# Kernel optimization log

Measured on AMD Instinct MI355X. Metric: run time of the kernel, lower is better.

## Reference

```python
import jax, jax.numpy as jnp
import numpy as np

N_WORDS = 8192   # total words across all concepts
L = 24           # chars per word (padded)
D = 256          # word_vec_d
H = 8            # attention heads
DFF = 1024
VOCAB = 128
N_CONCEPTS = 1024
MAXW = 16        # max_words
GROUPS = 4       # n_names: 4 equal groups of concepts


def setup_inputs() -> dict:
    key = jax.random.key(0)
    ks = jax.random.split(key, 9)
    rng = np.random.default_rng(0)
    # char tokens in [1, VOCAB), ragged word lengths in [4, L], tail = 0 (pad)
    vals = rng.integers(1, VOCAB, size=(N_WORDS, L))
    lens = rng.integers(4, L + 1, size=(N_WORDS,))
    inputs = np.where(np.arange(L)[None, :] < lens[:, None], vals, 0)
    # ragged words-per-concept: alternate 4 / 12 -> sums to N_WORDS, <= MAXW
    counts = np.where(np.arange(N_CONCEPTS) % 2 == 0, 4, 12)
    concept_id = np.repeat(np.arange(N_CONCEPTS), counts)
    word_pos = np.concatenate([np.arange(c) for c in counts])

    def w(k, shape):
        return 0.02 * jax.random.normal(k, shape, jnp.float32)

    return {
        "inputs": jnp.asarray(inputs, jnp.int32),
        "concept_id": jnp.asarray(concept_id, jnp.int32),
        "word_pos": jnp.asarray(word_pos, jnp.int32),
        "n_concepts": N_CONCEPTS,
        "n_names": GROUPS,
        "we_emb": w(ks[0], (VOCAB, D)),
        "we_qkv": w(ks[1], (D, 3 * D)),
        "we_o": w(ks[2], (D, D)),
        "we_ff1": w(ks[3], (D, DFF)),
        "we_ff2": w(ks[4], (DFF, D)),
        "ne_qkv": w(ks[5], (D, 3 * D)),
        "ne_o": w(ks[6], (D, D)),
        "ne_ff1": w(ks[7], (D, DFF)),
        "ne_ff2": w(ks[8], (DFF, D)),
    }


def _ln(x):
    m = x.mean(-1, keepdims=True)
    v = ((x - m) ** 2).mean(-1, keepdims=True)
    return (x - m) * jax.lax.rsqrt(v + 1e-5)


def _mha(x, wqkv, wo, key_pad=None):
    n, l, d = x.shape
    hd = d // H
    q, k, v = jnp.split(x @ wqkv, 3, axis=-1)
    q = q.reshape(n, l, H, hd)
    k = k.reshape(n, l, H, hd)
    v = v.reshape(n, l, H, hd)
    s = jnp.einsum('nqhd,nkhd->nhqk', q, k) / jnp.sqrt(jnp.asarray(hd, x.dtype))
    if key_pad is not None:
        s = jnp.where(key_pad[:, None, None, :], -1e9, s)
    a = jax.nn.softmax(s, axis=-1)
    o = jnp.einsum('nhqk,nkhd->nqhd', a, v).reshape(n, l, d)
    return o @ wo


def _block(x, wqkv, wo, w1, w2, key_pad=None):
    h = _ln(x + _mha(x, wqkv, wo, key_pad))
    return _ln(h + jax.nn.relu(h @ w1) @ w2)


def reference(inputs, concept_id, word_pos, n_concepts, n_names,
              we_emb, we_qkv, we_o, we_ff1, we_ff2,
              ne_qkv, ne_o, ne_ff1, ne_ff2):
    pad_mask = inputs == 0  # [N_WORDS, L]
    x = we_emb[inputs]      # [N_WORDS, L, D]
    word_ft = _block(x, we_qkv, we_o, we_ff1, we_ff2, pad_mask)
    # masked mean over chars -> one vector per word
    np_mask = (~pad_mask)[..., None].astype(word_ft.dtype)  # [N_WORDS, L, 1]
    name_vec = (word_ft * np_mask).sum(1) / np_mask.sum(1)   # [N_WORDS, D]
    # ragged -> padded: one scatter instead of per-sample torch.cat
    padded = jnp.zeros((n_concepts, MAXW, name_vec.shape[-1]), name_vec.dtype)
    padded = padded.at[concept_id, word_pos].set(name_vec)   # [n_concepts, MAXW, D]
    name_ft = _block(padded, ne_qkv, ne_o, ne_ff1, ne_ff2)
    row_pad = (padded == 0).all(-1, keepdims=True)           # all-zero rows = pad words
    name_ft = jnp.where(row_pad, jnp.zeros((), name_ft.dtype), name_ft)
    counts = (name_ft != 0).sum(1).astype(name_ft.dtype)     # [n_concepts, D]
    pooled = name_ft.sum(1) / counts                         # [n_concepts, D]
    return tuple(jnp.split(pooled, n_names, axis=0))
```

## Files before the change

### kernel.cpp

```cpp
#include <hip/hip_runtime.h>
#include <hip/hip_bf16.h>

#define NWORDS 8192
#define LW 24
#define DIM 256
#define NHEAD 8
#define DFF 1024
#define NCONC 1024
#define MAXW 16
#define TN (NCONC * MAXW)

typedef float floatx4 __attribute__((ext_vector_type(4)));
typedef short shortx8 __attribute__((ext_vector_type(8)));

__device__ __forceinline__ float bf2f(ushort u) {
  union { uint u; float f; } v; v.u = ((uint)u) << 16; return v.f;
}
__device__ __forceinline__ ushort f2bf(float f) {
  union { float f; uint u; } v; v.f = f;
  return (ushort)((v.u + 0x7FFFu + ((v.u >> 16) & 1u)) >> 16);
}

__device__ __forceinline__ void load_lds16(const ushort* gsrc, ushort* lds) {
  __builtin_amdgcn_global_load_lds((const __attribute__((address_space(1))) void*)gsrc,
                                   (__attribute__((address_space(3))) void*)lds, 16, 0, 0);
}

#define WAIT_VM0() __builtin_amdgcn_s_waitcnt(0x0F70)
#define WAIT_LGKM0() __builtin_amdgcn_s_waitcnt(0xC07F)

#define STAGE_COL(lane) ((((lane) & 3) ^ (((lane) >> 3) & 3)) * 8)
#define FRAG_OFF(row, quad) (((row) * 32) + ((((quad) ^ (((row) >> 1) & 3))) * 8))

__global__ __launch_bounds__(256) void wprep(const float* __restrict__ W,
                                             ushort* __restrict__ WT, int K, int N) {
  int idx = blockIdx.x * 256 + threadIdx.x;
  if (idx < K * N) {
    int k = idx / N, n = idx % N;
    WT[n * K + k] = f2bf(W[idx]);
  }
}

__global__ __launch_bounds__(256) void embed4(const int* __restrict__ inputs,
                                              const float* __restrict__ we_emb,
                                              ushort* __restrict__ x, int ntok) {
  int idx = blockIdx.x * 256 + threadIdx.x;
  int t = idx >> 6, d = (idx & 63) * 4;
  if (t < ntok) {
    const float4 f = *(const float4*)&we_emb[inputs[t] * DIM + d];
    uint2 o;
    o.x = (uint)f2bf(f.x) | ((uint)f2bf(f.y) << 16);
    o.y = (uint)f2bf(f.z) | ((uint)f2bf(f.w) << 16);
    *(uint2*)&x[(size_t)t * DIM + d] = o;
  }
}

template <bool LN>
__global__ __launch_bounds__(256, 2) void gemm_tok64(const ushort* __restrict__ A, int lda,
                                                     const ushort* __restrict__ BT,
                                                     const ushort* __restrict__ RES,
                                                     ushort* __restrict__ C, int ldc) {
  __shared__ __align__(16) ushort As[8 * 64 * 32];
  __shared__ __align__(16) ushort Wb[256 * 32];
  __shared__ float red1[64 * 4];
  __shared__ float red2[64 * 4];
  const int tid = threadIdx.x;
  const int w = tid >> 6, lane = tid & 63;
  const int quad = lane >> 4, l16 = lane & 15;
  const long m0 = (long)blockIdx.y * 64;
  const long nb = (long)blockIdx.x * 256;
  const int srow = lane >> 2;
  const int scol = STAGE_COL(lane);
  const int wc = w * 64;

#pragma unroll
  for (int t = 0; t < 8; t++) {
    int p = 2 * w + t / 4, ii = t % 4;
    load_lds16(&A[(m0 + ii * 16 + srow) * lda + p * 32 + scol], &As[p * 2048 + (ii * 16) * 32]);
  }
#pragma unroll
  for (int ii = 0; ii < 4; ii++)
    load_lds16(&BT[(nb + wc + ii * 16 + srow) * 256 + scol], &Wb[(wc + ii * 16) * 32]);
  __syncthreads();

  floatx4 acc[4][4] = {};
#pragma unroll 1
  for (int p = 0; p < 8; p++) {
    WAIT_VM0();
    shortx8 a[4], b[4];
#pragma unroll
    for (int j = 0; j < 4; j++)
      b[j] = *(const shortx8*)&Wb[FRAG_OFF(wc + j * 16 + l16, quad)];
    WAIT_LGKM0();
    if (p < 7) {
#pragma unroll
      for (int ii = 0; ii < 4; ii++)
        load_lds16(&BT[(nb + wc + ii * 16 + srow) * 256 + (p + 1) * 32 + scol],
                   &Wb[(wc + ii * 16) * 32]);
    }
#pragma unroll
    for (int i = 0; i < 4; i++)
      a[i] = *(const shortx8*)&As[p * 2048 + FRAG_OFF(i * 16 + l16, quad)];
#pragma unroll
    for (int i = 0; i < 4; i++)
#pragma unroll
      for (int j = 0; j < 4; j++)
        acc[i][j] = __builtin_amdgcn_mfma_f32_16x16x32_bf16(a[i], b[j], acc[i][j], 0, 0, 0);
  }

  if (!LN) {
#pragma unroll
    for (int i = 0; i < 4; i++)
#pragma unroll
      for (int j = 0; j < 4; j++)
#pragma unroll
        for (int r = 0; r < 4; r++) {
          long m = m0 + i * 16 + quad * 4 + r;
          C[m * ldc + nb + wc + j * 16 + l16] = f2bf(acc[i][j][r]);
        }
    return;
  }

#pragma unroll
  for (int i = 0; i < 4; i++)
#pragma unroll
    for (int r = 0; r < 4; r++) {
      int row = i * 16 + quad * 4 + r;
      float s1 = 0.f, s2 = 0.f;
#pragma unroll
      for (int j = 0; j < 4; j++) {
        float v = acc[i][j][r] + bf2f(RES[(m0 + row) * 256 + wc + j * 16 + l16]);
        acc[i][j][r] = v;
        s1 += v;
        s2 += v * v;
      }
#pragma unroll
      for (int off = 1; off < 16; off <<= 1) {
        s1 += __shfl_xor(s1, off);
        s2 += __shfl_xor(s2, off);
      }
      if (l16 == 0) { red1[row * 4 + w] = s1; red2[row * 4 + w] = s2; }
    }
  __syncthreads();
#pragma unroll
  for (int i = 0; i < 4; i++)
#pragma unroll
    for (int r = 0; r < 4; r++) {
      int row = i * 16 + quad * 4 + r;
      float s1 = red1[row * 4] + red1[row * 4 + 1] + red1[row * 4 + 2] + red1[row * 4 + 3];
      float s2 = red2[row * 4] + red2[row * 4 + 1] + red2[row * 4 + 2] + red2[row * 4 + 3];
      float mean = s1 * (1.f / 256.f);
      float rstd = rsqrtf(s2 * (1.f / 256.f) - mean * mean + 1e-5f);
#pragma unroll
      for (int j = 0; j < 4; j++)
        C[(m0 + row) * 256 + wc + j * 16 + l16] = f2bf((acc[i][j][r] - mean) * rstd);
    }
}

__global__ __launch_bounds__(256, 2) void ffn_fused(const ushort* __restrict__ H,
                                                    const ushort* __restrict__ W1T,
                                                    const ushort* __restrict__ W2T,
                                                    ushort* __restrict__ C,
                                                    int M) {
  __shared__ __align__(16) ushort As[8 * 64 * 32];
  __shared__ __align__(16) ushort Ss[8 * 64 * 32];
  __shared__ __align__(16) ushort Wb[256 * 32];
  const int tid = threadIdx.x;
  const int w = tid >> 6, lane = tid & 63;
  const int quad = lane >> 4, l16 = lane & 15;
  const long m0 = (long)blockIdx.x * 64;
  const int srow = lane >> 2;
  const int scol = STAGE_COL(lane);

#pragma unroll
  for (int t = 0; t < 8; t++) {
    int p = 2 * w + t / 4, ii = t % 4;
    load_lds16(&H[(m0 + ii * 16 + srow) * 256 + p * 32 + scol], &As[(p * 2048) + (ii * 16) * 32]);
  }
#pragma unroll
  for (int ii = 0; ii < 4; ii++)
    load_lds16(&W1T[(long)(w * 64 + ii * 16 + srow) * 256 + scol], &Wb[(w * 64 + ii * 16) * 32]);
  __syncthreads();

  floatx4 acc2[4][4] = {};
  for (int m = 0; m < 4; m++) {
    floatx4 acc1[4][4] = {};
    if (m > 0) {
#pragma unroll
      for (int ii = 0; ii < 4; ii++)
        load_lds16(&W1T[(long)(m * 256 + w * 64 + ii * 16 + srow) * 256 + scol],
                   &Wb[(w * 64 + ii * 16) * 32]);
    }
#pragma unroll 1
    for (int p = 0; p < 8; p++) {
      WAIT_VM0();
      shortx8 a[4], b[4];
#pragma unroll
      for (int i = 0; i < 4; i++)
        a[i] = *(const shortx8*)&Wb[FRAG_OFF(w * 64 + i * 16 + l16, quad)];
      WAIT_LGKM0();
      if (p < 7) {
#pragma unroll
        for (int ii = 0; ii < 4; ii++)
          load_lds16(&W1T[(long)(m * 256 + w * 64 + ii * 16 + srow) * 256 + (p + 1) * 32 + scol],
                     &Wb[(w * 64 + ii * 16) * 32]);
      }
#pragma unroll
      for (int j = 0; j < 4; j++)
        b[j] = *(const shortx8*)&As[p * 2048 + FRAG_OFF(j * 16 + l16, quad)];
#pragma unroll
      for (int i = 0; i < 4; i++)
#pragma unroll
        for (int j = 0; j < 4; j++)
          acc1[i][j] = __builtin_amdgcn_mfma_f32_16x16x32_bf16(a[i], b[j], acc1[i][j], 0, 0, 0);
    }
    __syncthreads();
#pragma unroll
    for (int i = 0; i < 4; i++) {
      int fb = w * 64 + i * 16 + quad * 4;
      int pf = fb >> 5, c = (fb >> 3) & 3, off = fb & 7;
#pragma unroll
      for (int j = 0; j < 4; j++) {
        int tok = j * 16 + l16;
        ushort4 pk;
        pk.x = f2bf(fmaxf(acc1[i][j][0], 0.f));
        pk.y = f2bf(fmaxf(acc1[i][j][1], 0.f));
        pk.z = f2bf(fmaxf(acc1[i][j][2], 0.f));
        pk.w = f2bf(fmaxf(acc1[i][j][3], 0.f));
        *(ushort4*)&Ss[(pf * 64 + tok) * 32 + ((c ^ ((tok >> 1) & 3)) << 3) + off] = pk;
      }
    }
    __syncthreads();
#pragma unroll
    for (int jj = 0; jj < 4; jj++)
      load_lds16(&W2T[(long)(w * 64 + jj * 16 + srow) * 1024 + m * 256 + scol],
                 &Wb[(w * 64 + jj * 16) * 32]);
#pragma unroll 1
    for (int p = 0; p < 8; p++) {
      WAIT_VM0();
      shortx8 a[4], b[4];
#pragma unroll
      for (int j = 0; j < 4; j++)
        b[j] = *(const shortx8*)&Wb[FRAG_OFF(w * 64 + j * 16 + l16, quad)];
      WAIT_LGKM0();
      if (p < 7) {
#pragma unroll
        for (int jj = 0; jj < 4; jj++)
          load_lds16(&W2T[(long)(w * 64 + jj * 16 + srow) * 1024 + m * 256 + (p + 1) * 32 + scol],
                     &Wb[(w * 64 + jj * 16) * 32]);
      }
#pragma unroll
      for (int i = 0; i < 4; i++)
        a[i] = *(const shortx8*)&Ss[p * 2048 + FRAG_OFF(i * 16 + l16, quad)];
#pragma unroll
      for (int i = 0; i < 4; i++)
#pragma unroll
        for (int j = 0; j < 4; j++)
          acc2[i][j] = __builtin_amdgcn_mfma_f32_16x16x32_bf16(a[i], b[j], acc2[i][j], 0, 0, 0);
    }
  }
  __syncthreads();

  float* red1 = (float*)Ss;
  float* red2 = red1 + 256;
  const int wc = w * 64;
#pragma unroll
  for (int i = 0; i < 4; i++)
#pragma unroll
    for (int r = 0; r < 4; r++) {
      int row = i * 16 + quad * 4 + r;
      float s1 = 0.f, s2 = 0.f;
#pragma unroll
      for (int j = 0; j < 4; j++) {
        float v = acc2[i][j][r] + bf2f(H[(m0 + row) * 256 + wc + j * 16 + l16]);
        acc2[i][j][r] = v;
        s1 += v;
        s2 += v * v;
      }
#pragma unroll
      for (int off = 1; off < 16; off <<= 1) {
        s1 += __shfl_xor(s1, off);
        s2 += __shfl_xor(s2, off);
      }
      if (l16 == 0) { red1[row * 4 + w] = s1; red2[row * 4 + w] = s2; }
    }
  __syncthreads();
#pragma unroll
  for (int i = 0; i < 4; i++)
#pragma unroll
    for (int r = 0; r < 4; r++) {
      int row = i * 16 + quad * 4 + r;
      float s1 = red1[row * 4] + red1[row * 4 + 1] + red1[row * 4 + 2] + red1[row * 4 + 3];
      float s2 = red2[row * 4] + red2[row * 4 + 1] + red2[row * 4 + 2] + red2[row * 4 + 3];
      float mean = s1 * (1.f / 256.f);
      float rstd = rsqrtf(s2 * (1.f / 256.f) - mean * mean + 1e-5f);
      if (m0 + row < M) {
#pragma unroll
        for (int j = 0; j < 4; j++)
          C[(m0 + row) * 256 + wc + j * 16 + l16] = f2bf((acc2[i][j][r] - mean) * rstd);
      }
    }
}

template <int LSEQ, bool MASKED>
__global__ __launch_bounds__(256) void attn(const int* __restrict__ inputs,
                                            ushort* __restrict__ qkv) {
  __shared__ ushort Qs[LSEQ * 256];
  __shared__ ushort Ks[LSEQ * 256];
  __shared__ ushort Vs[LSEQ * 256];
  __shared__ float pads[LSEQ];
  const int blk = blockIdx.x;
  const int tid = threadIdx.x;
  ushort* base = qkv + (size_t)blk * LSEQ * 768;
  const uint4* src = (const uint4*)base;
  for (int i = tid; i < LSEQ * 96; i += 256) {
    int c = i / 96, part = i % 96;
    uint4 val = src[c * 96 + part];
    int sect = part >> 5, off = part & 31;
    ushort* dst = (sect == 0) ? Qs : (sect == 1 ? Ks : Vs);
    *(uint4*)&dst[c * 256 + off * 8] = val;
  }
  if (MASKED) {
    if (tid < LSEQ) pads[tid] = (inputs[blk * LSEQ + tid] == 0) ? 1.f : 0.f;
  }
  __syncthreads();
  if (tid < LSEQ * NHEAD) {
    const int i = tid % LSEQ, hh = tid / LSEQ;
    const int hb = hh * 32;
    float q[32];
    {
      const uint4* qr = (const uint4*)&Qs[i * 256 + hb];
#pragma unroll
      for (int u = 0; u < 4; u++) {
        uint4 ch = qr[u];
        const ushort* us = (const ushort*)&ch;
#pragma unroll
        for (int d = 0; d < 8; d++) q[u * 8 + d] = bf2f(us[d]);
      }
    }
    float s[LSEQ];
    float mx = -3e38f;
#pragma unroll
    for (int j = 0; j < LSEQ; j++) {
      const uint4* kr = (const uint4*)&Ks[j * 256 + hb];
      float a = 0.f;
#pragma unroll
      for (int u = 0; u < 4; u++) {
        uint4 ch = kr[u];
        const ushort* us = (const ushort*)&ch;
#pragma unroll
        for (int d = 0; d < 8; d++) a += q[u * 8 + d] * bf2f(us[d]);
      }
      a *= 0.17677669529663687f;
      if (MASKED && pads[j] != 0.f) a = -1e9f;
      s[j] = a;
      mx = fmaxf(mx, a);
    }
    float den = 0.f;
#pragma unroll
    for (int j = 0; j < LSEQ; j++) { s[j] = __expf(s[j] - mx); den += s[j]; }
    float inv = 1.f / den;
    float o[32] = {};
#pragma unroll
    for (int j = 0; j < LSEQ; j++) {
      float a = s[j] * inv;
      const uint4* vr = (const uint4*)&Vs[j * 256 + hb];
#pragma unroll
      for (int u = 0; u < 4; u++) {
        uint4 ch = vr[u];
        const ushort* us = (const ushort*)&ch;
#pragma unroll
        for (int d = 0; d < 8; d++) o[u * 8 + d] += a * bf2f(us[d]);
      }
    }
    ushort* orow = base + (size_t)i * 768 + hb;
#pragma unroll
    for (int d = 0; d < 32; d++) orow[d] = f2bf(o[d]);
  }
}

__global__ __launch_bounds__(256) void pool_scatter(const ushort* __restrict__ ft,
                                                    const int* __restrict__ inputs,
                                                    const int* __restrict__ cid,
                                                    const int* __restrict__ wpos,
                                                    ushort* __restrict__ padded,
                                                    int* __restrict__ flags) {
  int w = blockIdx.x, d = threadIdx.x;
  float s = 0.f;
  int cnt = 0;
  for (int c = 0; c < LW; c++) {
    if (inputs[w * LW + c] != 0) {
      s += bf2f(ft[((size_t)w * LW + c) * DIM + d]);
      cnt++;
    }
  }
  int slot = cid[w] * MAXW + wpos[w];
  padded[(size_t)slot * DIM + d] = f2bf(s / (float)cnt);
  if (d == 0) flags[slot] = 1;
}

__global__ __launch_bounds__(256) void final_pool(const ushort* __restrict__ nft,
                                                  const int* __restrict__ flags,
                                                  float* __restrict__ out) {
  int n = blockIdx.x, d = threadIdx.x;
  float s = 0.f;
  int cnt = 0;
  for (int wd = 0; wd < MAXW; wd++) {
    if (flags[n * MAXW + wd]) {
      s += bf2f(nft[((size_t)n * MAXW + wd) * DIM + d]);
      cnt++;
    }
  }
  out[n * DIM + d] = s / (float)cnt;
}

extern "C" void kernel_launch(void* const* d_in, const int* in_sizes, int n_in,
                              void* d_out, int out_size, void* d_ws, size_t ws_size,
                              hipStream_t stream) {
  const int* inputs = (const int*)d_in[0];
  const int* cid = (const int*)d_in[1];
  const int* wpos = (const int*)d_in[2];
  const float* we_emb = (const float*)d_in[5];
  const float* we_qkv = (const float*)d_in[6];
  const float* we_o = (const float*)d_in[7];
  const float* we_ff1 = (const float*)d_in[8];
  const float* we_ff2 = (const float*)d_in[9];
  const float* ne_qkv = (const float*)d_in[10];
  const float* ne_o = (const float*)d_in[11];
  const float* ne_ff1 = (const float*)d_in[12];
  const float* ne_ff2 = (const float*)d_in[13];
  float* out = (float*)d_out;

  int chunks = 4;
  if (ws_size >= 515000000UL) chunks = 1;
  else if (ws_size >= 263258112UL) chunks = 2;
  const int wpc = NWORDS / chunks;
  const int tpc = wpc * LW;

  const size_t X = (size_t)tpc * DIM * 2;
  const size_t Q = (size_t)tpc * 768 * 2;

  char* base = (char*)d_ws;
  ushort* x = (ushort*)(base);
  ushort* qkv = (ushort*)(base + X);
  ushort* h = (ushort*)(base + X + Q);
  ushort* ft = qkv;
  size_t pend = X + Q + X;
  ushort* padded = (ushort*)(base + pend);
  int* flags = (int*)(base + pend + 8388608);
  ushort* wT = (ushort*)(base + pend + 8454144);
  ushort* nqkv = (ushort*)(base);
  ushort* nh = (ushort*)(base + 25165824);
  ushort* nft = (ushort*)(base + 33554432);

  ushort* wqkvT = wT;
  ushort* woT = wT + 196608;
  ushort* wff1T = wT + 262144;
  ushort* wff2T = wT + 524288;
  ushort* nqkvT = wT + 786432;
  ushort* neoT = wT + 983040;
  ushort* neff1T = wT + 1048576;
  ushort* neff2T = wT + 1310720;

  wprep<<<768, 256, 0, stream>>>(we_qkv, wqkvT, 256, 768);
  wprep<<<256, 256, 0, stream>>>(we_o, woT, 256, 256);
  wprep<<<1024, 256, 0, stream>>>(we_ff1, wff1T, 256, 1024);
  wprep<<<1024, 256, 0, stream>>>(we_ff2, wff2T, 1024, 256);
  wprep<<<768, 256, 0, stream>>>(ne_qkv, nqkvT, 256, 768);
  wprep<<<256, 256, 0, stream>>>(ne_o, neoT, 256, 256);
  wprep<<<1024, 256, 0, stream>>>(ne_ff1, neff1T, 256, 1024);
  wprep<<<1024, 256, 0, stream>>>(ne_ff2, neff2T, 1024, 256);

  (void)hipMemsetAsync(padded, 0, (size_t)TN * DIM * 2, stream);
  (void)hipMemsetAsync(flags, 0, TN * 4, stream);

  for (int c = 0; c < chunks; c++) {
    const int* in_c = inputs + (size_t)c * wpc * LW;
    const int* cid_c = cid + (size_t)c * wpc;
    const int* wpos_c = wpos + (size_t)c * wpc;

    embed4<<<tpc / 4, 256, 0, stream>>>(in_c, we_emb, x, tpc);
    {
      dim3 g(3, tpc / 64);
      gemm_tok64<false><<<g, 256, 0, stream>>>(x, 256, wqkvT, nullptr, qkv, 768);
    }
    attn<24, true><<<wpc, 256, 0, stream>>>(in_c, qkv);
    {
      dim3 g(1, tpc / 64);
      gemm_tok64<true><<<g, 256, 0, stream>>>(qkv, 768, woT, x, h, 256);
    }
    ffn_fused<<<tpc / 64, 256, 0, stream>>>(h, wff1T, wff2T, ft, tpc);
    pool_scatter<<<wpc, 256, 0, stream>>>(ft, in_c, cid_c, wpos_c, padded, flags);
  }

  {
    dim3 g(3, TN / 64);
    gemm_tok64<false><<<g, 256, 0, stream>>>(padded, 256, nqkvT, nullptr, nqkv, 768);
  }
  attn<16, false><<<NCONC, 256, 0, stream>>>(nullptr, nqkv);
  {
    dim3 g(1, TN / 64);
    gemm_tok64<true><<<g, 256, 0, stream>>>(nqkv, 768, neoT, padded, nh, 256);
  }
  ffn_fused<<<TN / 64, 256, 0, stream>>>(nh, neff1T, neff2T, nft, TN);
  final_pool<<<NCONC, 256, 0, stream>>>(nft, flags, out);
}
```

Baseline: 972.8 us.

## Load FFN weight fragments directly into registers with double-buffered prefetch

The fused FFN kernel no longer stages W1/W2 weight tiles through a shared LDS buffer. Each wave now loads its own weight fragments straight from global memory into a two-slot register double buffer, prefetching two k-steps ahead across both GEMM phases and across m iterations. This drops the per-step vmcnt waits, the LDS writes and reads for weights, and some block-wide __syncthreads, which are replaced by raw s_barrier. In exchange it uses more VGPRs, issues uncoalesced 16-byte global loads, and fully unrolls the inner loops.

```diff
diff --git a/kernel.cpp b/kernel.cpp
--- a/kernel.cpp
+++ b/kernel.cpp
@@ -164,47 +164,42 @@
                                                     int M) {
   __shared__ __align__(16) ushort As[8 * 64 * 32];
   __shared__ __align__(16) ushort Ss[8 * 64 * 32];
-  __shared__ __align__(16) ushort Wb[256 * 32];
   const int tid = threadIdx.x;
   const int w = tid >> 6, lane = tid & 63;
   const int quad = lane >> 4, l16 = lane & 15;
   const long m0 = (long)blockIdx.x * 64;
   const int srow = lane >> 2;
   const int scol = STAGE_COL(lane);
+  const int wb = w * 64;
 
 #pragma unroll
   for (int t = 0; t < 8; t++) {
     int p = 2 * w + t / 4, ii = t % 4;
     load_lds16(&H[(m0 + ii * 16 + srow) * 256 + p * 32 + scol], &As[(p * 2048) + (ii * 16) * 32]);
   }
-#pragma unroll
-  for (int ii = 0; ii < 4; ii++)
-    load_lds16(&W1T[(long)(w * 64 + ii * 16 + srow) * 256 + scol], &Wb[(w * 64 + ii * 16) * 32]);
+
+  const ushort* w1w = W1T + ((long)(wb + l16)) * 256 + quad * 8;
+  const ushort* w2w = W2T + ((long)(wb + l16)) * 1024 + quad * 8;
+
+  shortx8 wreg[2][4];
+#define LDW1(s, mm, pp)                                                              \
+  { _Pragma("unroll") for (int ii = 0; ii < 4; ii++)                                 \
+      wreg[s][ii] = *(const shortx8*)&w1w[((long)((mm)*256 + ii * 16)) * 256 + (pp) * 32]; }
+#define LDW2(s, mm, pp)                                                              \
+  { _Pragma("unroll") for (int jj = 0; jj < 4; jj++)                                 \
+      wreg[s][jj] = *(const shortx8*)&w2w[(long)(jj * 16) * 1024 + (mm)*256 + (pp) * 32]; }
+
+  LDW1(0, 0, 0);
+  LDW1(1, 0, 1);
   __syncthreads();
 
   floatx4 acc2[4][4] = {};
+#pragma unroll 1
   for (int m = 0; m < 4; m++) {
     floatx4 acc1[4][4] = {};
-    if (m > 0) {
-#pragma unroll
-      for (int ii = 0; ii < 4; ii++)
-        load_lds16(&W1T[(long)(m * 256 + w * 64 + ii * 16 + srow) * 256 + scol],
-                   &Wb[(w * 64 + ii * 16) * 32]);
-    }
-#pragma unroll 1
+#pragma unroll
     for (int p = 0; p < 8; p++) {
-      WAIT_VM0();
-      shortx8 a[4], b[4];
-#pragma unroll
-      for (int i = 0; i < 4; i++)
-        a[i] = *(const shortx8*)&Wb[FRAG_OFF(w * 64 + i * 16 + l16, quad)];
-      WAIT_LGKM0();
-      if (p < 7) {
-#pragma unroll
-        for (int ii = 0; ii < 4; ii++)
-          load_lds16(&W1T[(long)(m * 256 + w * 64 + ii * 16 + srow) * 256 + (p + 1) * 32 + scol],
-                     &Wb[(w * 64 + ii * 16) * 32]);
-      }
+      shortx8 b[4];
 #pragma unroll
       for (int j = 0; j < 4; j++)
         b[j] = *(const shortx8*)&As[p * 2048 + FRAG_OFF(j * 16 + l16, quad)];
@@ -212,12 +207,15 @@
       for (int i = 0; i < 4; i++)
 #pragma unroll
         for (int j = 0; j < 4; j++)
-          acc1[i][j] = __builtin_amdgcn_mfma_f32_16x16x32_bf16(a[i], b[j], acc1[i][j], 0, 0, 0);
-    }
-    __syncthreads();
+          acc1[i][j] = __builtin_amdgcn_mfma_f32_16x16x32_bf16(wreg[p & 1][i], b[j], acc1[i][j], 0, 0, 0);
+      if (p < 6) { LDW1((p & 1), m, p + 2); }
+      else if (p == 6) { LDW2(0, m, 0); }
+      else { LDW2(1, m, 1); }
+    }
+    asm volatile("s_barrier" ::: "memory");
 #pragma unroll
     for (int i = 0; i < 4; i++) {
-      int fb = w * 64 + i * 16 + quad * 4;
+      int fb = wb + i * 16 + quad * 4;
       int pf = fb >> 5, c = (fb >> 3) & 3, off = fb & 7;
 #pragma unroll
       for (int j = 0; j < 4; j++) {
@@ -230,25 +228,11 @@
         *(ushort4*)&Ss[(pf * 64 + tok) * 32 + ((c ^ ((tok >> 1) & 3)) << 3) + off] = pk;
       }
     }
-    __syncthreads();
-#pragma unroll
-    for (int jj = 0; jj < 4; jj++)
-      load_lds16(&W2T[(long)(w * 64 + jj * 16 + srow) * 1024 + m * 256 + scol],
-                 &Wb[(w * 64 + jj * 16) * 32]);
-#pragma unroll 1
+    asm volatile("s_waitcnt lgkmcnt(0)" ::: "memory");
+    asm volatile("s_barrier" ::: "memory");
+#pragma unroll
     for (int p = 0; p < 8; p++) {
-      WAIT_VM0();
-      shortx8 a[4], b[4];
-#pragma unroll
-      for (int j = 0; j < 4; j++)
-        b[j] = *(const shortx8*)&Wb[FRAG_OFF(w * 64 + j * 16 + l16, quad)];
-      WAIT_LGKM0();
-      if (p < 7) {
-#pragma unroll
-        for (int jj = 0; jj < 4; jj++)
-          load_lds16(&W2T[(long)(w * 64 + jj * 16 + srow) * 1024 + m * 256 + (p + 1) * 32 + scol],
-                     &Wb[(w * 64 + jj * 16) * 32]);
-      }
+      shortx8 a[4];
 #pragma unroll
       for (int i = 0; i < 4; i++)
         a[i] = *(const shortx8*)&Ss[p * 2048 + FRAG_OFF(i * 16 + l16, quad)];
@@ -256,9 +240,16 @@
       for (int i = 0; i < 4; i++)
 #pragma unroll
         for (int j = 0; j < 4; j++)
-          acc2[i][j] = __builtin_amdgcn_mfma_f32_16x16x32_bf16(a[i], b[j], acc2[i][j], 0, 0, 0);
-    }
-  }
+          acc2[i][j] = __builtin_amdgcn_mfma_f32_16x16x32_bf16(a[i], wreg[p & 1][j], acc2[i][j], 0, 0, 0);
+      if (p < 6) { LDW2((p & 1), m, p + 2); }
+      else if (m < 3) {
+        if (p == 6) { LDW1(0, m + 1, 0); }
+        else { LDW1(1, m + 1, 1); }
+      }
+    }
+  }
+#undef LDW1
+#undef LDW2
   __syncthreads();
 
   float* red1 = (float*)Ss;
```

After: 1.115 ms. +14.7%, slower.

## Split GEMM and fused FFN work across eight waves per block

Applied to the files above, without the earlier changes.

The token GEMM and fused FFN kernels move from 4 to 8 wavefronts per block, each wave owning a 32-column slice instead of 64. Staging loads, fragment loads, accumulators and the LayerNorm cross-wave reduction are all resized for 8 partial sums. The aim is to cut per-wave accumulator registers and raise latency hiding and occupancy. In exchange each wave reuses its A fragments over fewer MFMAs, and the block pays more barrier and reduction overhead.

```diff
diff --git a/kernel.cpp b/kernel.cpp
--- a/kernel.cpp
+++ b/kernel.cpp
@@ -56,14 +56,14 @@
 }
 
 template <bool LN>
-__global__ __launch_bounds__(256, 2) void gemm_tok64(const ushort* __restrict__ A, int lda,
+__global__ __launch_bounds__(512, 4) void gemm_tok64(const ushort* __restrict__ A, int lda,
                                                      const ushort* __restrict__ BT,
                                                      const ushort* __restrict__ RES,
                                                      ushort* __restrict__ C, int ldc) {
   __shared__ __align__(16) ushort As[8 * 64 * 32];
   __shared__ __align__(16) ushort Wb[256 * 32];
-  __shared__ float red1[64 * 4];
-  __shared__ float red2[64 * 4];
+  __shared__ float red1[64 * 8];
+  __shared__ float red2[64 * 8];
   const int tid = threadIdx.x;
   const int w = tid >> 6, lane = tid & 63;
   const int quad = lane >> 4, l16 = lane & 15;
@@ -71,32 +71,32 @@
   const long nb = (long)blockIdx.x * 256;
   const int srow = lane >> 2;
   const int scol = STAGE_COL(lane);
-  const int wc = w * 64;
-
-#pragma unroll
-  for (int t = 0; t < 8; t++) {
-    int p = 2 * w + t / 4, ii = t % 4;
+  const int sb = w * 32;
+
+#pragma unroll
+  for (int t = 0; t < 4; t++) {
+    int idx = w * 4 + t, p = idx >> 2, ii = idx & 3;
     load_lds16(&A[(m0 + ii * 16 + srow) * lda + p * 32 + scol], &As[p * 2048 + (ii * 16) * 32]);
   }
 #pragma unroll
-  for (int ii = 0; ii < 4; ii++)
-    load_lds16(&BT[(nb + wc + ii * 16 + srow) * 256 + scol], &Wb[(wc + ii * 16) * 32]);
+  for (int ii = 0; ii < 2; ii++)
+    load_lds16(&BT[(nb + sb + ii * 16 + srow) * 256 + scol], &Wb[(sb + ii * 16) * 32]);
   __syncthreads();
 
-  floatx4 acc[4][4] = {};
+  floatx4 acc[4][2] = {};
 #pragma unroll 1
   for (int p = 0; p < 8; p++) {
     WAIT_VM0();
-    shortx8 a[4], b[4];
-#pragma unroll
-    for (int j = 0; j < 4; j++)
-      b[j] = *(const shortx8*)&Wb[FRAG_OFF(wc + j * 16 + l16, quad)];
+    shortx8 a[4], b[2];
+#pragma unroll
+    for (int j = 0; j < 2; j++)
+      b[j] = *(const shortx8*)&Wb[FRAG_OFF(sb + j * 16 + l16, quad)];
     WAIT_LGKM0();
     if (p < 7) {
 #pragma unroll
-      for (int ii = 0; ii < 4; ii++)
-        load_lds16(&BT[(nb + wc + ii * 16 + srow) * 256 + (p + 1) * 32 + scol],
-                   &Wb[(wc + ii * 16) * 32]);
+      for (int ii = 0; ii < 2; ii++)
+        load_lds16(&BT[(nb + sb + ii * 16 + srow) * 256 + (p + 1) * 32 + scol],
+                   &Wb[(sb + ii * 16) * 32]);
     }
 #pragma unroll
     for (int i = 0; i < 4; i++)
@@ -104,7 +104,7 @@
 #pragma unroll
     for (int i = 0; i < 4; i++)
 #pragma unroll
-      for (int j = 0; j < 4; j++)
+      for (int j = 0; j < 2; j++)
         acc[i][j] = __builtin_amdgcn_mfma_f32_16x16x32_bf16(a[i], b[j], acc[i][j], 0, 0, 0);
   }
 
@@ -112,11 +112,11 @@
 #pragma unroll
     for (int i = 0; i < 4; i++)
 #pragma unroll
-      for (int j = 0; j < 4; j++)
+      for (int j = 0; j < 2; j++)
 #pragma unroll
         for (int r = 0; r < 4; r++) {
           long m = m0 + i * 16 + quad * 4 + r;
-          C[m * ldc + nb + wc + j * 16 + l16] = f2bf(acc[i][j][r]);
+          C[m * ldc + nb + sb + j * 16 + l16] = f2bf(acc[i][j][r]);
         }
     return;
   }
@@ -128,8 +128,8 @@
       int row = i * 16 + quad * 4 + r;
       float s1 = 0.f, s2 = 0.f;
 #pragma unroll
-      for (int j = 0; j < 4; j++) {
-        float v = acc[i][j][r] + bf2f(RES[(m0 + row) * 256 + wc + j * 16 + l16]);
+      for (int j = 0; j < 2; j++) {
+        float v = acc[i][j][r] + bf2f(RES[(m0 + row) * 256 + sb + j * 16 + l16]);
         acc[i][j][r] = v;
         s1 += v;
         s2 += v * v;
@@ -139,7 +139,7 @@
         s1 += __shfl_xor(s1, off);
         s2 += __shfl_xor(s2, off);
       }
-      if (l16 == 0) { red1[row * 4 + w] = s1; red2[row * 4 + w] = s2; }
+      if (l16 == 0) { red1[row * 8 + w] = s1; red2[row * 8 + w] = s2; }
     }
   __syncthreads();
 #pragma unroll
@@ -147,17 +147,18 @@
 #pragma unroll
     for (int r = 0; r < 4; r++) {
       int row = i * 16 + quad * 4 + r;
-      float s1 = red1[row * 4] + red1[row * 4 + 1] + red1[row * 4 + 2] + red1[row * 4 + 3];
-      float s2 = red2[row * 4] + red2[row * 4 + 1] + red2[row * 4 + 2] + red2[row * 4 + 3];
+      float s1 = 0.f, s2 = 0.f;
+#pragma unroll
+      for (int k = 0; k < 8; k++) { s1 += red1[row * 8 + k]; s2 += red2[row * 8 + k]; }
       float mean = s1 * (1.f / 256.f);
       float rstd = rsqrtf(s2 * (1.f / 256.f) - mean * mean + 1e-5f);
 #pragma unroll
-      for (int j = 0; j < 4; j++)
-        C[(m0 + row) * 256 + wc + j * 16 + l16] = f2bf((acc[i][j][r] - mean) * rstd);
-    }
-}
-
-__global__ __launch_bounds__(256, 2) void ffn_fused(const ushort* __restrict__ H,
+      for (int j = 0; j < 2; j++)
+        C[(m0 + row) * 256 + sb + j * 16 + l16] = f2bf((acc[i][j][r] - mean) * rstd);
+    }
+}
+
+__global__ __launch_bounds__(512, 4) void ffn_fused(const ushort* __restrict__ H,
                                                     const ushort* __restrict__ W1T,
                                                     const ushort* __restrict__ W2T,
                                                     ushort* __restrict__ C,
@@ -171,53 +172,54 @@
   const long m0 = (long)blockIdx.x * 64;
   const int srow = lane >> 2;
   const int scol = STAGE_COL(lane);
-
-#pragma unroll
-  for (int t = 0; t < 8; t++) {
-    int p = 2 * w + t / 4, ii = t % 4;
+  const int sb = w * 32;
+
+#pragma unroll
+  for (int t = 0; t < 4; t++) {
+    int idx = w * 4 + t, p = idx >> 2, ii = idx & 3;
     load_lds16(&H[(m0 + ii * 16 + srow) * 256 + p * 32 + scol], &As[(p * 2048) + (ii * 16) * 32]);
   }
 #pragma unroll
-  for (int ii = 0; ii < 4; ii++)
-    load_lds16(&W1T[(long)(w * 64 + ii * 16 + srow) * 256 + scol], &Wb[(w * 64 + ii * 16) * 32]);
+  for (int ii = 0; ii < 2; ii++)
+    load_lds16(&W1T[(long)(sb + ii * 16 + srow) * 256 + scol], &Wb[(sb + ii * 16) * 32]);
   __syncthreads();
 
-  floatx4 acc2[4][4] = {};
+  floatx4 acc2[4][2] = {};
   for (int m = 0; m < 4; m++) {
-    floatx4 acc1[4][4] = {};
+    floatx4 acc1[2][4] = {};
     if (m > 0) {
 #pragma unroll
-      for (int ii = 0; ii < 4; ii++)
-        load_lds16(&W1T[(long)(m * 256 + w * 64 + ii * 16 + srow) * 256 + scol],
-                   &Wb[(w * 64 + ii * 16) * 32]);
+      for (int ii = 0; ii < 2; ii++)
+        load_lds16(&W1T[(long)(m * 256 + sb + ii * 16 + srow) * 256 + scol],
+                   &Wb[(sb + ii * 16) * 32]);
     }
 #pragma unroll 1
     for (int p = 0; p < 8; p++) {
       WAIT_VM0();
-      shortx8 a[4], b[4];
-#pragma unroll
-      for (int i = 0; i < 4; i++)
-        a[i] = *(const shortx8*)&Wb[FRAG_OFF(w * 64 + i * 16 + l16, quad)];
+      shortx8 a[2], b[4];
+#pragma unroll
+      for (int i = 0; i < 2; i++)
+        a[i] = *(const shortx8*)&Wb[FRAG_OFF(sb + i * 16 + l16, quad)];
       WAIT_LGKM0();
       if (p < 7) {
 #pragma unroll
-        for (int ii = 0; ii < 4; ii++)
-          load_lds16(&W1T[(long)(m * 256 + w * 64 + ii * 16 + srow) * 256 + (p + 1) * 32 + scol],
-                     &Wb[(w * 64 + ii * 16) * 32]);
+        for (int ii = 0; ii < 2; ii++)
+          load_lds16(&W1T[(long)(m * 256 + sb + ii * 16 + srow) * 256 + (p + 1) * 32 + scol],
+                     &Wb[(sb + ii * 16) * 32]);
       }
 #pragma unroll
       for (int j = 0; j < 4; j++)
         b[j] = *(const shortx8*)&As[p * 2048 + FRAG_OFF(j * 16 + l16, quad)];
 #pragma unroll
-      for (int i = 0; i < 4; i++)
+      for (int i = 0; i < 2; i++)
 #pragma unroll
         for (int j = 0; j < 4; j++)
           acc1[i][j] = __builtin_amdgcn_mfma_f32_16x16x32_bf16(a[i], b[j], acc1[i][j], 0, 0, 0);
     }
     __syncthreads();
 #pragma unroll
-    for (int i = 0; i < 4; i++) {
-      int fb = w * 64 + i * 16 + quad * 4;
+    for (int i = 0; i < 2; i++) {
+      int fb = sb + i * 16 + quad * 4;
       int pf = fb >> 5, c = (fb >> 3) & 3, off = fb & 7;
 #pragma unroll
       for (int j = 0; j < 4; j++) {
@@ -232,22 +234,22 @@
     }
     __syncthreads();
 #pragma unroll
-    for (int jj = 0; jj < 4; jj++)
-      load_lds16(&W2T[(long)(w * 64 + jj * 16 + srow) * 1024 + m * 256 + scol],
-                 &Wb[(w * 64 + jj * 16) * 32]);
+    for (int jj = 0; jj < 2; jj++)
+      load_lds16(&W2T[(long)(sb + jj * 16 + srow) * 1024 + m * 256 + scol],
+                 &Wb[(sb + jj * 16) * 32]);
 #pragma unroll 1
     for (int p = 0; p < 8; p++) {
       WAIT_VM0();
-      shortx8 a[4], b[4];
-#pragma unroll
-      for (int j = 0; j < 4; j++)
-        b[j] = *(const shortx8*)&Wb[FRAG_OFF(w * 64 + j * 16 + l16, quad)];
+      shortx8 a[4], b[2];
+#pragma unroll
+      for (int j = 0; j < 2; j++)
+        b[j] = *(const shortx8*)&Wb[FRAG_OFF(sb + j * 16 + l16, quad)];
       WAIT_LGKM0();
       if (p < 7) {
 #pragma unroll
-        for (int jj = 0; jj < 4; jj++)
-          load_lds16(&W2T[(long)(w * 64 + jj * 16 + srow) * 1024 + m * 256 + (p + 1) * 32 + scol],
-                     &Wb[(w * 64 + jj * 16) * 32]);
+        for (int jj = 0; jj < 2; jj++)
+          load_lds16(&W2T[(long)(sb + jj * 16 + srow) * 1024 + m * 256 + (p + 1) * 32 + scol],
+                     &Wb[(sb + jj * 16) * 32]);
       }
 #pragma unroll
       for (int i = 0; i < 4; i++)
@@ -255,15 +257,14 @@
 #pragma unroll
       for (int i = 0; i < 4; i++)
 #pragma unroll
-        for (int j = 0; j < 4; j++)
+        for (int j = 0; j < 2; j++)
           acc2[i][j] = __builtin_amdgcn_mfma_f32_16x16x32_bf16(a[i], b[j], acc2[i][j], 0, 0, 0);
     }
   }
   __syncthreads();
 
   float* red1 = (float*)Ss;
-  float* red2 = red1 + 256;
-  const int wc = w * 64;
+  float* red2 = red1 + 512;
 #pragma unroll
   for (int i = 0; i < 4; i++)
 #pragma unroll
@@ -271,8 +272,8 @@
       int row = i * 16 + quad * 4 + r;
       float s1 = 0.f, s2 = 0.f;
 #pragma unroll
-      for (int j = 0; j < 4; j++) {
-        float v = acc2[i][j][r] + bf2f(H[(m0 + row) * 256 + wc + j * 16 + l16]);
+      for (int j = 0; j < 2; j++) {
+        float v = acc2[i][j][r] + bf2f(H[(m0 + row) * 256 + sb + j * 16 + l16]);
         acc2[i][j][r] = v;
         s1 += v;
         s2 += v * v;
@@ -282,7 +283,7 @@
         s1 += __shfl_xor(s1, off);
         s2 += __shfl_xor(s2, off);
       }
-      if (l16 == 0) { red1[row * 4 + w] = s1; red2[row * 4 + w] = s2; }
+      if (l16 == 0) { red1[row * 8 + w] = s1; red2[row * 8 + w] = s2; }
     }
   __syncthreads();
 #pragma unroll
@@ -290,14 +291,15 @@
 #pragma unroll
     for (int r = 0; r < 4; r++) {
       int row = i * 16 + quad * 4 + r;
-      float s1 = red1[row * 4] + red1[row * 4 + 1] + red1[row * 4 + 2] + red1[row * 4 + 3];
-      float s2 = red2[row * 4] + red2[row * 4 + 1] + red2[row * 4 + 2] + red2[row * 4 + 3];
+      float s1 = 0.f, s2 = 0.f;
+#pragma unroll
+      for (int k = 0; k < 8; k++) { s1 += red1[row * 8 + k]; s2 += red2[row * 8 + k]; }
       float mean = s1 * (1.f / 256.f);
       float rstd = rsqrtf(s2 * (1.f / 256.f) - mean * mean + 1e-5f);
       if (m0 + row < M) {
 #pragma unroll
-        for (int j = 0; j < 4; j++)
-          C[(m0 + row) * 256 + wc + j * 16 + l16] = f2bf((acc2[i][j][r] - mean) * rstd);
+        for (int j = 0; j < 2; j++)
+          C[(m0 + row) * 256 + sb + j * 16 + l16] = f2bf((acc2[i][j][r] - mean) * rstd);
       }
     }
 }
@@ -482,26 +484,26 @@
     embed4<<<tpc / 4, 256, 0, stream>>>(in_c, we_emb, x, tpc);
     {
       dim3 g(3, tpc / 64);
-      gemm_tok64<false><<<g, 256, 0, stream>>>(x, 256, wqkvT, nullptr, qkv, 768);
+      gemm_tok64<false><<<g, 512, 0, stream>>>(x, 256, wqkvT, nullptr, qkv, 768);
     }
     attn<24, true><<<wpc, 256, 0, stream>>>(in_c, qkv);
     {
       dim3 g(1, tpc / 64);
-      gemm_tok64<true><<<g, 256, 0, stream>>>(qkv, 768, woT, x, h, 256);
-    }
-    ffn_fused<<<tpc / 64, 256, 0, stream>>>(h, wff1T, wff2T, ft, tpc);
+      gemm_tok64<true><<<g, 512, 0, stream>>>(qkv, 768, woT, x, h, 256);
+    }
+    ffn_fused<<<tpc / 64, 512, 0, stream>>>(h, wff1T, wff2T, ft, tpc);
     pool_scatter<<<wpc, 256, 0, stream>>>(ft, in_c, cid_c, wpos_c, padded, flags);
   }
 
   {
     dim3 g(3, TN / 64);
-    gemm_tok64<false><<<g, 256, 0, stream>>>(padded, 256, nqkvT, nullptr, nqkv, 768);
+    gemm_tok64<false><<<g, 512, 0, stream>>>(padded, 256, nqkvT, nullptr, nqkv, 768);
   }
   attn<16, false><<<NCONC, 256, 0, stream>>>(nullptr, nqkv);
   {
     dim3 g(1, TN / 64);
-    gemm_tok64<true><<<g, 256, 0, stream>>>(nqkv, 768, neoT, padded, nh, 256);
-  }
-  ffn_fused<<<TN / 64, 256, 0, stream>>>(nh, neff1T, neff2T, nft, TN);
+    gemm_tok64<true><<<g, 512, 0, stream>>>(nqkv, 768, neoT, padded, nh, 256);
+  }
+  ffn_fused<<<TN / 64, 512, 0, stream>>>(nh, neff1T, neff2T, nft, TN);
   final_pool<<<NCONC, 256, 0, stream>>>(nft, flags, out);
 }
```

After: 1.007 ms. 3.5% more time.

## Split fused FFN into separate FF1+ReLU GEMM and K=1024 GEMM with LayerNorm

Applied to the files above, without the earlier changes.

Replaces the fused FFN kernel, which kept the 1024-wide hidden activation in shared memory, with two kernels. The first is a ReLU-epilogue GEMM that writes the hidden activation to a global scratch buffer (split into halves for the word stage). The second is a K=1024 GEMM with residual add and LayerNorm. This spreads the first GEMM across four column blocks for more parallelism and avoids holding two accumulator sets per block. The cost is extra global memory traffic for the intermediate and more kernel launches.

```diff
diff --git a/kernel.cpp b/kernel.cpp
--- a/kernel.cpp
+++ b/kernel.cpp
@@ -55,7 +55,7 @@
   }
 }
 
-template <bool LN>
+template <bool LN, bool RELU>
 __global__ __launch_bounds__(256, 2) void gemm_tok64(const ushort* __restrict__ A, int lda,
                                                      const ushort* __restrict__ BT,
                                                      const ushort* __restrict__ RES,
@@ -116,7 +116,9 @@
 #pragma unroll
         for (int r = 0; r < 4; r++) {
           long m = m0 + i * 16 + quad * 4 + r;
-          C[m * ldc + nb + wc + j * 16 + l16] = f2bf(acc[i][j][r]);
+          float v = acc[i][j][r];
+          if (RELU) v = fmaxf(v, 0.f);
+          C[m * ldc + nb + wc + j * 16 + l16] = f2bf(v);
         }
     return;
   }
@@ -157,113 +159,63 @@
     }
 }
 
-__global__ __launch_bounds__(256, 2) void ffn_fused(const ushort* __restrict__ H,
-                                                    const ushort* __restrict__ W1T,
-                                                    const ushort* __restrict__ W2T,
-                                                    ushort* __restrict__ C,
-                                                    int M) {
+__global__ __launch_bounds__(256, 2) void gemm_k1024_ln(const ushort* __restrict__ A,
+                                                        const ushort* __restrict__ BT,
+                                                        const ushort* __restrict__ RES,
+                                                        ushort* __restrict__ C) {
   __shared__ __align__(16) ushort As[8 * 64 * 32];
-  __shared__ __align__(16) ushort Ss[8 * 64 * 32];
   __shared__ __align__(16) ushort Wb[256 * 32];
+  __shared__ float red1[64 * 4];
+  __shared__ float red2[64 * 4];
   const int tid = threadIdx.x;
   const int w = tid >> 6, lane = tid & 63;
   const int quad = lane >> 4, l16 = lane & 15;
   const long m0 = (long)blockIdx.x * 64;
   const int srow = lane >> 2;
   const int scol = STAGE_COL(lane);
-
-#pragma unroll
-  for (int t = 0; t < 8; t++) {
-    int p = 2 * w + t / 4, ii = t % 4;
-    load_lds16(&H[(m0 + ii * 16 + srow) * 256 + p * 32 + scol], &As[(p * 2048) + (ii * 16) * 32]);
-  }
-#pragma unroll
-  for (int ii = 0; ii < 4; ii++)
-    load_lds16(&W1T[(long)(w * 64 + ii * 16 + srow) * 256 + scol], &Wb[(w * 64 + ii * 16) * 32]);
-  __syncthreads();
-
-  floatx4 acc2[4][4] = {};
-  for (int m = 0; m < 4; m++) {
-    floatx4 acc1[4][4] = {};
-    if (m > 0) {
-#pragma unroll
-      for (int ii = 0; ii < 4; ii++)
-        load_lds16(&W1T[(long)(m * 256 + w * 64 + ii * 16 + srow) * 256 + scol],
-                   &Wb[(w * 64 + ii * 16) * 32]);
-    }
+  const int wc = w * 64;
+
+  floatx4 acc[4][4] = {};
+#pragma unroll 1
+  for (int kc = 0; kc < 4; kc++) {
+#pragma unroll
+    for (int t = 0; t < 8; t++) {
+      int p = 2 * w + t / 4, ii = t % 4;
+      load_lds16(&A[(m0 + ii * 16 + srow) * 1024 + kc * 256 + p * 32 + scol],
+                 &As[p * 2048 + (ii * 16) * 32]);
+    }
+#pragma unroll
+    for (int ii = 0; ii < 4; ii++)
+      load_lds16(&BT[(long)(wc + ii * 16 + srow) * 1024 + kc * 256 + scol],
+                 &Wb[(wc + ii * 16) * 32]);
+    __syncthreads();
+
 #pragma unroll 1
     for (int p = 0; p < 8; p++) {
       WAIT_VM0();
       shortx8 a[4], b[4];
 #pragma unroll
-      for (int i = 0; i < 4; i++)
-        a[i] = *(const shortx8*)&Wb[FRAG_OFF(w * 64 + i * 16 + l16, quad)];
+      for (int j = 0; j < 4; j++)
+        b[j] = *(const shortx8*)&Wb[FRAG_OFF(wc + j * 16 + l16, quad)];
       WAIT_LGKM0();
       if (p < 7) {
 #pragma unroll
         for (int ii = 0; ii < 4; ii++)
-          load_lds16(&W1T[(long)(m * 256 + w * 64 + ii * 16 + srow) * 256 + (p + 1) * 32 + scol],
-                     &Wb[(w * 64 + ii * 16) * 32]);
-      }
-#pragma unroll
-      for (int j = 0; j < 4; j++)
-        b[j] = *(const shortx8*)&As[p * 2048 + FRAG_OFF(j * 16 + l16, quad)];
+          load_lds16(&BT[(long)(wc + ii * 16 + srow) * 1024 + kc * 256 + (p + 1) * 32 + scol],
+                     &Wb[(wc + ii * 16) * 32]);
+      }
 #pragma unroll
       for (int i = 0; i < 4; i++)
+        a[i] = *(const shortx8*)&As[p * 2048 + FRAG_OFF(i * 16 + l16, quad)];
+#pragma unroll
+      for (int i = 0; i < 4; i++)
 #pragma unroll
         for (int j = 0; j < 4; j++)
-          acc1[i][j] = __builtin_amdgcn_mfma_f32_16x16x32_bf16(a[i], b[j], acc1[i][j], 0, 0, 0);
+          acc[i][j] = __builtin_amdgcn_mfma_f32_16x16x32_bf16(a[i], b[j], acc[i][j], 0, 0, 0);
     }
     __syncthreads();
-#pragma unroll
-    for (int i = 0; i < 4; i++) {
-      int fb = w * 64 + i * 16 + quad * 4;
-      int pf = fb >> 5, c = (fb >> 3) & 3, off = fb & 7;
-#pragma unroll
-      for (int j = 0; j < 4; j++) {
-        int tok = j * 16 + l16;
-        ushort4 pk;
-        pk.x = f2bf(fmaxf(acc1[i][j][0], 0.f));
-        pk.y = f2bf(fmaxf(acc1[i][j][1], 0.f));
-        pk.z = f2bf(fmaxf(acc1[i][j][2], 0.f));
-        pk.w = f2bf(fmaxf(acc1[i][j][3], 0.f));
-        *(ushort4*)&Ss[(pf * 64 + tok) * 32 + ((c ^ ((tok >> 1) & 3)) << 3) + off] = pk;
-      }
-    }
-    __syncthreads();
-#pragma unroll
-    for (int jj = 0; jj < 4; jj++)
-      load_lds16(&W2T[(long)(w * 64 + jj * 16 + srow) * 1024 + m * 256 + scol],
-                 &Wb[(w * 64 + jj * 16) * 32]);
-#pragma unroll 1
-    for (int p = 0; p < 8; p++) {
-      WAIT_VM0();
-      shortx8 a[4], b[4];
-#pragma unroll
-      for (int j = 0; j < 4; j++)
-        b[j] = *(const shortx8*)&Wb[FRAG_OFF(w * 64 + j * 16 + l16, quad)];
-      WAIT_LGKM0();
-      if (p < 7) {
-#pragma unroll
-        for (int jj = 0; jj < 4; jj++)
-          load_lds16(&W2T[(long)(w * 64 + jj * 16 + srow) * 1024 + m * 256 + (p + 1) * 32 + scol],
-                     &Wb[(w * 64 + jj * 16) * 32]);
-      }
-#pragma unroll
-      for (int i = 0; i < 4; i++)
-        a[i] = *(const shortx8*)&Ss[p * 2048 + FRAG_OFF(i * 16 + l16, quad)];
-#pragma unroll
-      for (int i = 0; i < 4; i++)
-#pragma unroll
-        for (int j = 0; j < 4; j++)
-          acc2[i][j] = __builtin_amdgcn_mfma_f32_16x16x32_bf16(a[i], b[j], acc2[i][j], 0, 0, 0);
-    }
-  }
-  __syncthreads();
-
-  float* red1 = (float*)Ss;
-  float* red2 = red1 + 256;
-  const int wc = w * 64;
+  }
+
 #pragma unroll
   for (int i = 0; i < 4; i++)
 #pragma unroll
@@ -272,8 +224,8 @@
       float s1 = 0.f, s2 = 0.f;
 #pragma unroll
       for (int j = 0; j < 4; j++) {
-        float v = acc2[i][j][r] + bf2f(H[(m0 + row) * 256 + wc + j * 16 + l16]);
-        acc2[i][j][r] = v;
+        float v = acc[i][j][r] + bf2f(RES[(m0 + row) * 256 + wc + j * 16 + l16]);
+        acc[i][j][r] = v;
         s1 += v;
         s2 += v * v;
       }
@@ -294,11 +246,9 @@
       float s2 = red2[row * 4] + red2[row * 4 + 1] + red2[row * 4 + 2] + red2[row * 4 + 3];
       float mean = s1 * (1.f / 256.f);
       float rstd = rsqrtf(s2 * (1.f / 256.f) - mean * mean + 1e-5f);
-      if (m0 + row < M) {
-#pragma unroll
-        for (int j = 0; j < 4; j++)
-          C[(m0 + row) * 256 + wc + j * 16 + l16] = f2bf((acc2[i][j][r] - mean) * rstd);
-      }
+#pragma unroll
+      for (int j = 0; j < 4; j++)
+        C[(m0 + row) * 256 + wc + j * 16 + l16] = f2bf((acc[i][j][r] - mean) * rstd);
     }
 }
 
@@ -445,6 +395,7 @@
   ushort* qkv = (ushort*)(base + X);
   ushort* h = (ushort*)(base + X + Q);
   ushort* ft = qkv;
+  ushort* S = (ushort*)(base + 2 * X);
   size_t pend = X + Q + X;
   ushort* padded = (ushort*)(base + pend);
   int* flags = (int*)(base + pend + 8388608);
@@ -452,6 +403,7 @@
   ushort* nqkv = (ushort*)(base);
   ushort* nh = (ushort*)(base + 25165824);
   ushort* nft = (ushort*)(base + 33554432);
+  ushort* Sn = (ushort*)(base + 41943040);
 
   ushort* wqkvT = wT;
   ushort* woT = wT + 196608;
@@ -482,26 +434,39 @@
     embed4<<<tpc / 4, 256, 0, stream>>>(in_c, we_emb, x, tpc);
     {
       dim3 g(3, tpc / 64);
-      gemm_tok64<false><<<g, 256, 0, stream>>>(x, 256, wqkvT, nullptr, qkv, 768);
+      gemm_tok64<false, false><<<g, 256, 0, stream>>>(x, 256, wqkvT, nullptr, qkv, 768);
     }
     attn<24, true><<<wpc, 256, 0, stream>>>(in_c, qkv);
     {
       dim3 g(1, tpc / 64);
-      gemm_tok64<true><<<g, 256, 0, stream>>>(qkv, 768, woT, x, h, 256);
-    }
-    ffn_fused<<<tpc / 64, 256, 0, stream>>>(h, wff1T, wff2T, ft, tpc);
+      gemm_tok64<true, false><<<g, 256, 0, stream>>>(qkv, 768, woT, x, h, 256);
+    }
+    const int mh = tpc / 2;
+    for (int half = 0; half < 2; half++) {
+      const ushort* hh = h + (size_t)half * mh * 256;
+      ushort* fth = ft + (size_t)half * mh * 256;
+      {
+        dim3 g(4, mh / 64);
+        gemm_tok64<false, true><<<g, 256, 0, stream>>>(hh, 256, wff1T, nullptr, S, 1024);
+      }
+      gemm_k1024_ln<<<mh / 64, 256, 0, stream>>>(S, wff2T, hh, fth);
+    }
     pool_scatter<<<wpc, 256, 0, stream>>>(ft, in_c, cid_c, wpos_c, padded, flags);
   }
 
   {
     dim3 g(3, TN / 64);
-    gemm_tok64<false><<<g, 256, 0, stream>>>(padded, 256, nqkvT, nullptr, nqkv, 768);
+    gemm_tok64<false, false><<<g, 256, 0, stream>>>(padded, 256, nqkvT, nullptr, nqkv, 768);
   }
   attn<16, false><<<NCONC, 256, 0, stream>>>(nullptr, nqkv);
   {
     dim3 g(1, TN / 64);
-    gemm_tok64<true><<<g, 256, 0, stream>>>(nqkv, 768, neoT, padded, nh, 256);
-  }
-  ffn_fused<<<TN / 64, 256, 0, stream>>>(nh, neff1T, neff2T, nft, TN);
+    gemm_tok64<true, false><<<g, 256, 0, stream>>>(nqkv, 768, neoT, padded, nh, 256);
+  }
+  {
+    dim3 g(4, TN / 64);
+    gemm_tok64<false, true><<<g, 256, 0, stream>>>(nh, 256, neff1T, nullptr, Sn, 1024);
+  }
+  gemm_k1024_ln<<<TN / 64, 256, 0, stream>>>(Sn, neff2T, nh, nft);
   final_pool<<<NCONC, 256, 0, stream>>>(nft, flags, out);
 }
```

New measurement: 1.105 ms. 13.6% more time.
